# Optimization experiments

Hardware: AMD Instinct MI355X
Metric: run time of the kernel (lower is better)

## Reference

```python
import jax, jax.numpy as jnp
import numpy as np

N_NODES = 100000
N_EDGES = 300000
N_GRAPHS = 128
NODE_VOCAB = 200
NODE_DIM = 128
EDGE_VOCAB = 8
EDGE_DIM = 64
K_LAYERS = 3


def setup_inputs() -> dict:
    key = jax.random.key(0)
    ks = iter(jax.random.split(key, 40))
    f = lambda shape: jax.random.normal(next(ks), shape, dtype=jnp.float32)
    s = lambda shape: f(shape) * 0.05
    inp = {}
    inp["x_s"] = f((N_NODES, NODE_VOCAB))
    inp["x_t"] = f((N_NODES, NODE_VOCAB))
    inp["edge_attr_s"] = f((2 * N_EDGES, EDGE_VOCAB))
    inp["edge_attr_t"] = f((2 * N_EDGES, EDGE_VOCAB))
    inp["edge_index_s"] = jax.random.randint(next(ks), (2, N_EDGES), 0, N_NODES)
    inp["edge_index_t"] = jax.random.randint(next(ks), (2, N_EDGES), 0, N_NODES)
    inp["x_s_batch"] = jnp.sort(jax.random.randint(next(ks), (N_NODES,), 0, N_GRAPHS))
    inp["x_t_batch"] = jnp.sort(jax.random.randint(next(ks), (N_NODES,), 0, N_GRAPHS))
    inp["y"] = jax.random.randint(next(ks), (N_GRAPHS,), 0, 2)
    cat = 2 * NODE_DIM + EDGE_DIM  # 320: [x_src, edge_attr, x_dst]
    inp["node_emb"] = s((NODE_VOCAB, NODE_DIM))
    inp["edge_emb"] = s((EDGE_VOCAB, EDGE_DIM))
    inp["W_in_0"] = s((K_LAYERS, cat, EDGE_DIM))
    inp["W_in_1"] = s((K_LAYERS, EDGE_DIM, 1))
    inp["W_out_0"] = s((K_LAYERS, cat, EDGE_DIM))
    inp["W_out_1"] = s((K_LAYERS, EDGE_DIM, 1))
    inp["Wg_in"] = s((K_LAYERS, NODE_DIM, NODE_DIM))
    inp["bg_in"] = jnp.zeros((K_LAYERS, NODE_DIM), jnp.float32)
    inp["Wg_out"] = s((K_LAYERS, NODE_DIM, NODE_DIM))
    inp["bg_out"] = jnp.zeros((K_LAYERS, NODE_DIM), jnp.float32)
    inp["cls_W0"] = s((2 * NODE_DIM, NODE_DIM))
    inp["cls_b0"] = jnp.zeros((NODE_DIM,), jnp.float32)
    inp["cls_W1"] = s((NODE_DIM, 2))
    inp["cls_b1"] = jnp.zeros((2,), jnp.float32)
    return inp


def _dag_embed(x, e, row, col, W_in_0, W_in_1, W_out_0, W_out_1, Wg_in, bg_in, Wg_out, bg_out):
    N = x.shape[0]
    E = row.shape[0]
    for k in range(W_in_0.shape[0]):
        e_in, e_out = e[:E], e[E:]  # chunk(edge_attr_x, 2, dim=0)
        info_in = jnp.concatenate([x[row], e_in, x[col]], axis=1)   # [E, 2D+Ce]
        info_out = jnp.concatenate([x[col], e_out, x[row]], axis=1)
        e_in = info_in @ W_in_0[k]
        e_out = info_out @ W_out_0[k]
        w_in = jax.nn.sigmoid(e_in @ W_in_1[k]).ravel()   # [E]
        w_out = jax.nn.sigmoid(e_out @ W_out_1[k]).ravel()
        # embedding_in: flow source->target (x_j = x[row], aggregate at col)
        xi = x @ Wg_in[k]
        x_in = jax.ops.segment_sum(w_in[:, None] * xi[row], col, num_segments=N) + bg_in[k]
        # embedding_out: flow target->source (x_j = x[col], aggregate at row)
        xo = x @ Wg_out[k]
        x_out = jax.ops.segment_sum(w_out[:, None] * xo[col], row, num_segments=N) + bg_out[k]
        x = x + x_in + x_out
        e = jnp.concatenate([e_in, e_out], axis=0)
    return x


def _mean_pool(x, batch, num_graphs):
    sums = jax.ops.segment_sum(x, batch, num_segments=num_graphs)
    cnt = jax.ops.segment_sum(jnp.ones((x.shape[0], 1), x.dtype), batch, num_segments=num_graphs)
    return sums / jnp.maximum(cnt, 1.0)


def reference(x_s, x_t, edge_attr_s, edge_attr_t, edge_index_s, edge_index_t,
              x_s_batch, x_t_batch, y, node_emb, edge_emb,
              W_in_0, W_in_1, W_out_0, W_out_1, Wg_in, bg_in, Wg_out, bg_out,
              cls_W0, cls_b0, cls_W1, cls_b1):
    # Initialization: argmax -> embedding lookup
    h_s = node_emb[jnp.argmax(x_s, axis=1)]
    h_t = node_emb[jnp.argmax(x_t, axis=1)]
    he_s = edge_emb[jnp.argmax(edge_attr_s, axis=1)]
    he_t = edge_emb[jnp.argmax(edge_attr_t, axis=1)]
    h_s = _dag_embed(h_s, he_s, edge_index_s[0], edge_index_s[1],
                     W_in_0, W_in_1, W_out_0, W_out_1, Wg_in, bg_in, Wg_out, bg_out)
    h_t = _dag_embed(h_t, he_t, edge_index_t[0], edge_index_t[1],
                     W_in_0, W_in_1, W_out_0, W_out_1, Wg_in, bg_in, Wg_out, bg_out)
    g_s = _mean_pool(h_s, x_s_batch, N_GRAPHS)
    g_t = _mean_pool(h_t, x_t_batch, N_GRAPHS)
    h = jax.nn.relu(jnp.concatenate([g_s, g_t], axis=1) @ cls_W0 + cls_b0)
    logits = h @ cls_W1 + cls_b1
    logp = jax.nn.log_softmax(logits, axis=1)
    loss = -jnp.mean(jnp.take_along_axis(logp, y[:, None], axis=1))
    return loss
```

## Files before the change

kernel.cpp:

```cpp
#include <hip/hip_runtime.h>
#include <hip/hip_bf16.h>

#define N_NODES 100000
#define N_EDGES 300000
#define N_GRAPHS 128
#define NODE_VOCAB 200
#define NODE_DIM 128
#define EDGE_DIM 64
#define K_LAYERS 3

#define SCAN_CHUNK 2048
#define SCAN_NBLK ((N_NODES + SCAN_CHUNK - 1) / SCAN_CHUNK)

typedef unsigned short ushort_t;
typedef __attribute__((ext_vector_type(8))) __bf16 bf16x8;
typedef __attribute__((ext_vector_type(4))) float f32x4;

__device__ inline ushort_t f2bf(float f) {
    unsigned int u = __float_as_uint(f);
    unsigned int r = (u + 0x7fff + ((u >> 16) & 1)) >> 16;
    return (ushort_t)r;
}
__device__ inline float bf2f(ushort_t u) {
    return __uint_as_float(((unsigned int)u) << 16);
}
__device__ inline float bflo(unsigned int u) { return __uint_as_float(u << 16); }
__device__ inline float bfhi(unsigned int u) { return __uint_as_float(u & 0xffff0000u); }

#define MASK_J0 0x15151515u
#define MASK_J1 0x28282828u
#define MASK_J2 0x40404040u

__device__ ushort_t g_hb[2][(size_t)N_NODES * NODE_DIM];
__device__ ushort_t g_XWx_b[(size_t)N_NODES * 256];
__device__ ushort_t g_WcatT[256 * 128];
__device__ ushort_t g_QT[K_LAYERS][32][128];
__device__ float g_scal[(size_t)N_NODES * 32];
__device__ float g_bias[8][6];
__device__ int  g_evoc[2 * N_EDGES];
__device__ float g_gsum[2][N_GRAPHS * NODE_DIM];
__device__ float g_cnt[2][N_GRAPHS];
__device__ float g_H[N_GRAPHS * NODE_DIM];
__device__ int  g_deg_in[N_NODES];
__device__ int  g_deg_out[N_NODES];
__device__ int  g_off_in[N_NODES + 1];
__device__ int  g_off_out[N_NODES + 1];
__device__ int  g_cur_in[N_NODES];
__device__ int  g_cur_out[N_NODES];
__device__ int2 g_lst_in[N_EDGES];
__device__ int2 g_lst_out[N_EDGES];
__device__ int  g_bsum[2][SCAN_NBLK];
__device__ int  g_boff[2][SCAN_NBLK];

__global__ void node_embed_kernel(const float* __restrict__ x, const float* __restrict__ emb,
                                  int N) {
    int wave = threadIdx.x >> 6;
    int lane = threadIdx.x & 63;
    int n = blockIdx.x * 4 + wave;
    if (n >= N) return;
    const float* xr = x + (size_t)n * NODE_VOCAB;
    float v = xr[lane];
    int idx = lane;
    float nv = xr[lane + 64];
    if (nv > v) { v = nv; idx = lane + 64; }
    nv = xr[lane + 128];
    if (nv > v) { v = nv; idx = lane + 128; }
    if (lane < NODE_VOCAB - 192) {
        nv = xr[lane + 192];
        if (nv > v) { v = nv; idx = lane + 192; }
    }
    #pragma unroll
    for (int off = 32; off; off >>= 1) {
        float ov = __shfl_xor(v, off);
        int oi = __shfl_xor(idx, off);
        if (ov > v || (ov == v && oi < idx)) { v = ov; idx = oi; }
    }
    const float* er = emb + (size_t)idx * NODE_DIM;
    g_hb[0][(size_t)n * NODE_DIM + lane] = f2bf(er[lane]);
    g_hb[0][(size_t)n * NODE_DIM + 64 + lane] = f2bf(er[64 + lane]);
}

__global__ void edge_voc_kernel(const float* __restrict__ ea, int M) {
    long idx = (long)blockIdx.x * 256 + threadIdx.x;
    if (idx >= M) return;
    const float* ar = ea + idx * 8;
    float4 v0 = *(const float4*)ar;
    float4 v1 = *(const float4*)(ar + 4);
    float vals[8] = {v0.x, v0.y, v0.z, v0.w, v1.x, v1.y, v1.z, v1.w};
    int best = 0;
    float bv = vals[0];
    #pragma unroll
    for (int i = 1; i < 8; ++i)
        if (vals[i] > bv) { bv = vals[i]; best = i; }
    g_evoc[idx] = best;
}

__global__ void zero_qt_kernel() {
    int i = blockIdx.x * 256 + threadIdx.x;
    if (i < K_LAYERS * 32 * 128) ((ushort_t*)g_QT)[i] = 0;
}

__global__ void setup_gates_kernel(const float* __restrict__ Wi0, const float* __restrict__ Wi1,
                                   const float* __restrict__ Wo0, const float* __restrict__ Wo1,
                                   const float* __restrict__ eemb) {
    int b = blockIdx.x;
    int D = b / 3, k = b % 3;
    int t = threadIdx.x;
    const float* W0 = D ? Wo0 : Wi0;
    const float* W1 = D ? Wo1 : Wi1;
    __shared__ float u[64], un[64];
    if (t < 64) u[t] = W1[k * 64 + t];
    __syncthreads();
    int offk = (k == 0) ? 0 : (k == 1 ? 2 : 4);
    for (int j = k; j >= 0; --j) {
        const float* Wj = W0 + (size_t)j * 320 * 64;
        float qa = 0.f, qc = 0.f;
        for (int m = 0; m < 64; ++m) {
            float um = u[m];
            qa += Wj[t * 64 + m] * um;
            qc += Wj[(192 + t) * 64 + m] * um;
        }
        g_QT[j][(D ? 8 : 0) + offk + j][t] = f2bf(qa);
        g_QT[j][(D ? 24 : 16) + offk + j][t] = f2bf(qc);
        float s = 0.f;
        if (t < 64) {
            for (int m = 0; m < 64; ++m) s += Wj[(128 + t) * 64 + m] * u[m];
        }
        __syncthreads();
        if (t < 64) un[t] = s;
        __syncthreads();
        if (t < 64) u[t] = un[t];
        __syncthreads();
    }
    if (t < 8) {
        float s = 0.f;
        for (int m = 0; m < 64; ++m) s += eemb[t * 64 + m] * u[m];
        g_bias[t][D * 3 + k] = s;
    }
}

__global__ void csr_zero_kernel() {
    int i = blockIdx.x * 256 + threadIdx.x;
    if (i < N_NODES) { g_deg_in[i] = 0; g_deg_out[i] = 0; }
}

__global__ void csr_count_kernel(const int* __restrict__ row, const int* __restrict__ col,
                                 int E) {
    int e = blockIdx.x * 256 + threadIdx.x;
    if (e >= E) return;
    atomicAdd(&g_deg_in[col[e]], 1);
    atomicAdd(&g_deg_out[row[e]], 1);
}

__global__ void csr_bsum_kernel() {
    int which = blockIdx.y;
    const int* deg = which ? g_deg_out : g_deg_in;
    int b = blockIdx.x;
    int t = threadIdx.x;
    int base = b * SCAN_CHUNK;
    int s = 0;
    #pragma unroll
    for (int i = 0; i < SCAN_CHUNK / 256; ++i) {
        int idx = base + i * 256 + t;
        if (idx < N_NODES) s += deg[idx];
    }
    __shared__ int red[256];
    red[t] = s;
    __syncthreads();
    for (int d = 128; d; d >>= 1) {
        if (t < d) red[t] += red[t + d];
        __syncthreads();
    }
    if (t == 0) g_bsum[which][b] = red[0];
}

__global__ void csr_bscan_kernel() {
    int which = blockIdx.x;
    int t = threadIdx.x;
    int v = (t < SCAN_NBLK) ? g_bsum[which][t] : 0;
    int orig = v;
    #pragma unroll
    for (int d = 1; d < 64; d <<= 1) {
        int u = __shfl_up(v, d, 64);
        if (t >= d) v += u;
    }
    if (t < SCAN_NBLK) g_boff[which][t] = v - orig;
}

__global__ void csr_off_kernel(int total) {
    int which = blockIdx.y;
    const int* deg = which ? g_deg_out : g_deg_in;
    int* off = which ? g_off_out : g_off_in;
    int* cur = which ? g_cur_out : g_cur_in;
    int b = blockIdx.x;
    int t = threadIdx.x;
    const int per = SCAN_CHUNK / 256;
    int lo = b * SCAN_CHUNK + t * per;
    int d8[per];
    int s = 0;
    #pragma unroll
    for (int i = 0; i < per; ++i) {
        int idx = lo + i;
        d8[i] = (idx < N_NODES) ? deg[idx] : 0;
        s += d8[i];
    }
    __shared__ int part[256];
    part[t] = s;
    __syncthreads();
    for (int d = 1; d < 256; d <<= 1) {
        int add = (t >= d) ? part[t - d] : 0;
        __syncthreads();
        part[t] += add;
        __syncthreads();
    }
    int run = g_boff[which][b] + part[t] - s;
    #pragma unroll
    for (int i = 0; i < per; ++i) {
        int idx = lo + i;
        if (idx < N_NODES) {
            off[idx] = run;
            cur[idx] = run;
            run += d8[i];
        }
    }
    if (b == 0 && t == 0) off[N_NODES] = total;
}

__global__ void csr_fill_kernel(const int* __restrict__ row, const int* __restrict__ col,
                                int E) {
    int e = blockIdx.x * 256 + threadIdx.x;
    if (e >= E) return;
    int r = row[e], c = col[e];
    int p = atomicAdd(&g_cur_in[c], 1);
    g_lst_in[p] = make_int2(r, g_evoc[e]);
    int q = atomicAdd(&g_cur_out[r], 1);
    g_lst_out[q] = make_int2(c, g_evoc[E + e]);
}

__global__ void assemble_wcat(const float* __restrict__ Wgi, const float* __restrict__ Wgo) {
    int idx = blockIdx.x * 256 + threadIdx.x;
    int n = idx >> 7;
    int kd = idx & 127;
    float v = (n < 128) ? Wgi[kd * 128 + n] : Wgo[kd * 128 + (n - 128)];
    g_WcatT[n * 128 + kd] = f2bf(v);
}

__global__ __launch_bounds__(320) void gemm_xw_mfma(int cur, int layer, unsigned int mask,
                                                    int M) {
    const ushort_t* __restrict__ hb = g_hb[cur];
    int m0 = blockIdx.x * 64;
    int t = threadIdx.x;
    int wave = t >> 6, lane = t & 63;
    __shared__ ushort_t As[64 * 128];

    for (int idx = t; idx < 1024; idx += 320) {
        int m = idx >> 4, c = idx & 15;
        int gm = m0 + m;
        uint4 v = make_uint4(0u, 0u, 0u, 0u);
        if (gm < M) v = *(const uint4*)(hb + (size_t)gm * 128 + c * 8);
        *(uint4*)&As[m * 128 + ((c * 8) ^ ((m & 7) << 3))] = v;
    }
    __syncthreads();

    int lr = lane & 15, lk = lane >> 4;

    if (wave < 4) {
        int nbase = wave * 64;
        f32x4 acc[4][4];
        #pragma unroll
        for (int i = 0; i < 4; ++i)
            #pragma unroll
            for (int j = 0; j < 4; ++j)
                acc[i][j] = (f32x4){0.f, 0.f, 0.f, 0.f};

        const ushort_t* Bbase = g_WcatT + (size_t)nbase * 128;
        #pragma unroll
        for (int ks = 0; ks < 4; ++ks) {
            bf16x8 a[4], b[4];
            int ke = ks * 32 + lk * 8;
            #pragma unroll
            for (int mt = 0; mt < 4; ++mt) {
                int row = mt * 16 + lr;
                a[mt] = *(const bf16x8*)&As[row * 128 + (ke ^ ((row & 7) << 3))];
            }
            #pragma unroll
            for (int nt = 0; nt < 4; ++nt) {
                b[nt] = *(const bf16x8*)(Bbase + (size_t)(nt * 16 + lr) * 128 + ke);
            }
            #pragma unroll
            for (int nt = 0; nt < 4; ++nt)
                #pragma unroll
                for (int mt = 0; mt < 4; ++mt)
                    acc[nt][mt] = __builtin_amdgcn_mfma_f32_16x16x32_bf16(b[nt], a[mt], acc[nt][mt], 0, 0, 0);
        }

        #pragma unroll
        for (int mt = 0; mt < 4; ++mt) {
            int gm = m0 + mt * 16 + lr;
            if (gm >= M) continue;
            #pragma unroll
            for (int nt = 0; nt < 4; ++nt) {
                int n0 = nbase + nt * 16 + lk * 4;
                f32x4 av = acc[nt][mt];
                uint2 pk;
                pk.x = ((unsigned int)f2bf(av[1]) << 16) | (unsigned int)f2bf(av[0]);
                pk.y = ((unsigned int)f2bf(av[3]) << 16) | (unsigned int)f2bf(av[2]);
                *(uint2*)&g_XWx_b[(size_t)gm * 256 + n0] = pk;
            }
        }
    } else {
        const ushort_t* QT = &g_QT[layer][0][0];
        f32x4 acc[2][4];
        #pragma unroll
        for (int i = 0; i < 2; ++i)
            #pragma unroll
            for (int j = 0; j < 4; ++j)
                acc[i][j] = (f32x4){0.f, 0.f, 0.f, 0.f};

        #pragma unroll
        for (int ks = 0; ks < 4; ++ks) {
            bf16x8 a[4], b[2];
            int ke = ks * 32 + lk * 8;
            #pragma unroll
            for (int mt = 0; mt < 4; ++mt) {
                int row = mt * 16 + lr;
                a[mt] = *(const bf16x8*)&As[row * 128 + (ke ^ ((row & 7) << 3))];
            }
            #pragma unroll
            for (int nt = 0; nt < 2; ++nt)
                b[nt] = *(const bf16x8*)&QT[(nt * 16 + lr) * 128 + ke];
            #pragma unroll
            for (int nt = 0; nt < 2; ++nt)
                #pragma unroll
                for (int mt = 0; mt < 4; ++mt)
                    acc[nt][mt] = __builtin_amdgcn_mfma_f32_16x16x32_bf16(b[nt], a[mt], acc[nt][mt], 0, 0, 0);
        }

        #pragma unroll
        for (int mt = 0; mt < 4; ++mt) {
            int gm = m0 + mt * 16 + lr;
            if (gm >= M) continue;
            #pragma unroll
            for (int nt = 0; nt < 2; ++nt) {
                #pragma unroll
                for (int r = 0; r < 4; ++r) {
                    int colc = nt * 16 + lk * 4 + r;
                    if ((mask >> colc) & 1u)
                        g_scal[(size_t)gm * 32 + colc] = acc[nt][mt][r];
                }
            }
        }
    }
}

__global__ __launch_bounds__(256) void aggregate_kernel(int cur, int k,
                                                        const float* __restrict__ bgi,
                                                        const float* __restrict__ bgo, int N) {
    __shared__ float sW[4][64];
    __shared__ int sS[4][64];
    int wv = threadIdx.x >> 6;
    int lane = threadIdx.x & 63;
    int grp = lane >> 4, li = lane & 15;
    int n = blockIdx.x * 4 + wv;
    if (n >= N) return;
    float bias_in = g_bias[lane & 7][k];
    float bias_out = g_bias[lane & 7][3 + k];
    const float* srow = g_scal + (size_t)n * 32;
    float cin, cout;
    if (k == 0) {
        cin = srow[16]; cout = srow[24];
    } else if (k == 1) {
        cin = srow[18] + srow[19]; cout = srow[26] + srow[27];
    } else {
        cin = srow[20] + srow[21] + srow[22];
        cout = srow[28] + srow[29] + srow[30];
    }
    int pin0 = g_off_in[n], din = g_off_in[n + 1] - pin0;
    int pout0 = g_off_out[n], dout = g_off_out[n + 1] - pout0;
    int tot = din + dout;

    float acc[8];
    if (grp == 0) {
        uint4 xv = *(const uint4*)(g_hb[cur] + (size_t)n * 128 + li * 8);
        float4 b1 = *(const float4*)(bgi + li * 8);
        float4 b2 = *(const float4*)(bgi + li * 8 + 4);
        float4 c1 = *(const float4*)(bgo + li * 8);
        float4 c2 = *(const float4*)(bgo + li * 8 + 4);
        acc[0] = bflo(xv.x) + b1.x + c1.x;
        acc[1] = bfhi(xv.x) + b1.y + c1.y;
        acc[2] = bflo(xv.y) + b1.z + c1.z;
        acc[3] = bfhi(xv.y) + b1.w + c1.w;
        acc[4] = bflo(xv.z) + b2.x + c2.x;
        acc[5] = bfhi(xv.z) + b2.y + c2.y;
        acc[6] = bflo(xv.w) + b2.z + c2.z;
        acc[7] = bfhi(xv.w) + b2.w + c2.w;
    } else {
        #pragma unroll
        for (int q = 0; q < 8; ++q) acc[q] = 0.f;
    }

    for (int base = 0; base < tot; base += 64) {
        int cnt = min(64, tot - base);
        if (lane < cnt) {
            int q = base + lane;
            int2 se;
            int dir;
            if (q < din) { se = g_lst_in[pin0 + q]; dir = 0; }
            else         { se = g_lst_out[pout0 + q - din]; dir = 1; }
            const float* arow = g_scal + (size_t)se.x * 32 + dir * 8;
            float asum;
            if (k == 0) asum = arow[0];
            else if (k == 1) asum = arow[2] + arow[3];
            else asum = arow[4] + arow[5] + arow[6];
            float bi = __shfl(bias_in, se.y);
            float bo = __shfl(bias_out, se.y);
            float s = (dir ? bo : bi) + asum + (dir ? cout : cin);
            sW[wv][lane] = 1.0f / (1.0f + __expf(-s));
            sS[wv][lane] = se.x * 2 + dir;
        }
        for (int e = grp; e < cnt; e += 4) {
            float wvv = sW[wv][e];
            int sv = sS[wv][e];
            const ushort_t* src = g_XWx_b + (size_t)(sv >> 1) * 256 + (sv & 1) * 128 + li * 8;
            uint4 pv = *(const uint4*)src;
            acc[0] += wvv * bflo(pv.x);
            acc[1] += wvv * bfhi(pv.x);
            acc[2] += wvv * bflo(pv.y);
            acc[3] += wvv * bfhi(pv.y);
            acc[4] += wvv * bflo(pv.z);
            acc[5] += wvv * bfhi(pv.z);
            acc[6] += wvv * bflo(pv.w);
            acc[7] += wvv * bfhi(pv.w);
        }
    }
    #pragma unroll
    for (int q = 0; q < 8; ++q) {
        acc[q] += __shfl_xor(acc[q], 16);
        acc[q] += __shfl_xor(acc[q], 32);
    }
    if (grp == 0) {
        uint4 pk;
        pk.x = ((unsigned int)f2bf(acc[1]) << 16) | (unsigned int)f2bf(acc[0]);
        pk.y = ((unsigned int)f2bf(acc[3]) << 16) | (unsigned int)f2bf(acc[2]);
        pk.z = ((unsigned int)f2bf(acc[5]) << 16) | (unsigned int)f2bf(acc[4]);
        pk.w = ((unsigned int)f2bf(acc[7]) << 16) | (unsigned int)f2bf(acc[6]);
        *(uint4*)(g_hb[cur ^ 1] + (size_t)n * 128 + li * 8) = pk;
    }
}

__global__ void pool_kernel(int fin, int side, const int* __restrict__ batch, int N) {
    const ushort_t* x = g_hb[fin];
    float* gsum = g_gsum[side];
    int n0 = blockIdx.x * 128;
    int d = threadIdx.x;
    if (n0 >= N) return;
    int nend = min(n0 + 128, N);
    float acc = 0.f;
    int curg = batch[n0];
    for (int n = n0; n < nend; ++n) {
        int g = batch[n];
        if (g != curg) {
            atomicAdd(&gsum[curg * 128 + d], acc);
            acc = 0.f;
            curg = g;
        }
        acc += bf2f(x[(size_t)n * 128 + d]);
    }
    atomicAdd(&gsum[curg * 128 + d], acc);
}

__global__ void count_kernel(int side, const int* __restrict__ batch, int N) {
    int g = threadIdx.x;
    int lo = 0, hi = N;
    while (lo < hi) { int mid = (lo + hi) >> 1; if (batch[mid] < g) lo = mid + 1; else hi = mid; }
    int a = lo;
    lo = 0; hi = N;
    while (lo < hi) { int mid = (lo + hi) >> 1; if (batch[mid] < g + 1) lo = mid + 1; else hi = mid; }
    g_cnt[side][g] = (float)(lo - a);
}

__global__ void zero_gsum_kernel() {
    int i = blockIdx.x * 256 + threadIdx.x;
    if (i < 2 * N_GRAPHS * NODE_DIM) ((float*)g_gsum)[i] = 0.f;
}

__global__ void hidden_kernel(const float* __restrict__ W0, const float* __restrict__ b0) {
    int g = blockIdx.x;
    int j = threadIdx.x;
    float inv_s = 1.0f / fmaxf(g_cnt[0][g], 1.0f);
    float inv_t = 1.0f / fmaxf(g_cnt[1][g], 1.0f);
    float acc = b0[j];
    for (int k = 0; k < 128; ++k) acc += g_gsum[0][g * 128 + k] * inv_s * W0[k * 128 + j];
    for (int k = 0; k < 128; ++k) acc += g_gsum[1][g * 128 + k] * inv_t * W0[(128 + k) * 128 + j];
    g_H[g * 128 + j] = fmaxf(acc, 0.f);
}

__global__ void loss_kernel(const float* __restrict__ W1, const float* __restrict__ b1,
                            const int* __restrict__ y, float* __restrict__ out) {
    int g = threadIdx.x;
    float l0 = b1[0], l1 = b1[1];
    for (int j = 0; j < 128; ++j) {
        float hv = g_H[g * 128 + j];
        l0 += hv * W1[j * 2 + 0];
        l1 += hv * W1[j * 2 + 1];
    }
    float m = fmaxf(l0, l1);
    float lse = m + logf(expf(l0 - m) + expf(l1 - m));
    float ly = (y[g] == 0) ? l0 : l1;
    float c = -(ly - lse) * (1.0f / (float)N_GRAPHS);
    __shared__ float red[128];
    red[g] = c;
    __syncthreads();
    for (int s = 64; s; s >>= 1) {
        if (g < s) red[g] += red[g + s];
        __syncthreads();
    }
    if (g == 0) out[0] = red[0];
}

extern "C" void kernel_launch(void* const* d_in, const int* in_sizes, int n_in,
                              void* d_out, int out_size, void* d_ws, size_t ws_size,
                              hipStream_t stream) {
    const float* x_s      = (const float*)d_in[0];
    const float* x_t      = (const float*)d_in[1];
    const float* ea_s     = (const float*)d_in[2];
    const float* ea_t     = (const float*)d_in[3];
    const int*   ei_s     = (const int*)d_in[4];
    const int*   ei_t     = (const int*)d_in[5];
    const int*   batch_s  = (const int*)d_in[6];
    const int*   batch_t  = (const int*)d_in[7];
    const int*   y        = (const int*)d_in[8];
    const float* node_emb = (const float*)d_in[9];
    const float* edge_emb = (const float*)d_in[10];
    const float* W_in_0   = (const float*)d_in[11];
    const float* W_in_1   = (const float*)d_in[12];
    const float* W_out_0  = (const float*)d_in[13];
    const float* W_out_1  = (const float*)d_in[14];
    const float* Wg_in    = (const float*)d_in[15];
    const float* bg_in    = (const float*)d_in[16];
    const float* Wg_out   = (const float*)d_in[17];
    const float* bg_out   = (const float*)d_in[18];
    const float* cls_W0   = (const float*)d_in[19];
    const float* cls_b0   = (const float*)d_in[20];
    const float* cls_W1   = (const float*)d_in[21];
    const float* cls_b1   = (const float*)d_in[22];

    const int N = N_NODES, E = N_EDGES;
    static const unsigned int MASKS[3] = {MASK_J0, MASK_J1, MASK_J2};

    zero_gsum_kernel<<<(2 * N_GRAPHS * NODE_DIM + 255) / 256, 256, 0, stream>>>();
    zero_qt_kernel<<<(K_LAYERS * 32 * 128 + 255) / 256, 256, 0, stream>>>();
    setup_gates_kernel<<<6, 128, 0, stream>>>(W_in_0, W_in_1, W_out_0, W_out_1, edge_emb);

    for (int side = 0; side < 2; ++side) {
        const float* xin   = side ? x_t : x_s;
        const float* eain  = side ? ea_t : ea_s;
        const int*   ei    = side ? ei_t : ei_s;
        const int*   batch = side ? batch_t : batch_s;
        const int* row = ei;
        const int* col = ei + E;

        node_embed_kernel<<<(N + 3) / 4, 256, 0, stream>>>(xin, node_emb, N);
        edge_voc_kernel<<<(2 * E + 255) / 256, 256, 0, stream>>>(eain, 2 * E);

        csr_zero_kernel<<<(N + 255) / 256, 256, 0, stream>>>();
        csr_count_kernel<<<(E + 255) / 256, 256, 0, stream>>>(row, col, E);
        csr_bsum_kernel<<<dim3(SCAN_NBLK, 2), 256, 0, stream>>>();
        csr_bscan_kernel<<<2, 64, 0, stream>>>();
        csr_off_kernel<<<dim3(SCAN_NBLK, 2), 256, 0, stream>>>(E);
        csr_fill_kernel<<<(E + 255) / 256, 256, 0, stream>>>(row, col, E);

        int cur = 0;
        for (int k = 0; k < K_LAYERS; ++k) {
            assemble_wcat<<<128, 256, 0, stream>>>(Wg_in + (size_t)k * 128 * 128,
                                                   Wg_out + (size_t)k * 128 * 128);
            gemm_xw_mfma<<<(N + 63) / 64, 320, 0, stream>>>(cur, k, MASKS[k], N);
            aggregate_kernel<<<(N + 3) / 4, 256, 0, stream>>>(
                cur, k, bg_in + (size_t)k * 128, bg_out + (size_t)k * 128, N);
            cur ^= 1;
        }
        pool_kernel<<<(N + 127) / 128, 128, 0, stream>>>(cur, side, batch, N);
        count_kernel<<<1, 128, 0, stream>>>(side, batch, N);
    }

    hidden_kernel<<<128, 128, 0, stream>>>(cls_W0, cls_b0);
    loss_kernel<<<1, 128, 0, stream>>>(cls_W1, cls_b1, y, (float*)d_out);
}
```

Measured before the change: 922.4 us.

## Map one node per 16-lane group in aggregation and hoist weight assembly

The aggregation kernel now gives each node a 16-lane group instead of a whole wavefront, so four nodes share one wave. Gates are computed per lane and broadcast with shuffles instead of going through shared memory, and the final cross-group reduction goes away. The Wcat transpose for all layers is also built once up front rather than re-launched per layer and per side. The aim is better lane use on low-degree nodes and fewer launches, at the cost of divergence when node degrees differ within a wave.

```diff
diff --git a/kernel.cpp b/kernel.cpp
--- a/kernel.cpp
+++ b/kernel.cpp
@@ -33,7 +33,7 @@
 
 __device__ ushort_t g_hb[2][(size_t)N_NODES * NODE_DIM];
 __device__ ushort_t g_XWx_b[(size_t)N_NODES * 256];
-__device__ ushort_t g_WcatT[256 * 128];
+__device__ ushort_t g_WcatT[K_LAYERS][256 * 128];
 __device__ ushort_t g_QT[K_LAYERS][32][128];
 __device__ float g_scal[(size_t)N_NODES * 32];
 __device__ float g_bias[8][6];
@@ -237,12 +237,16 @@
     g_lst_out[q] = make_int2(c, g_evoc[E + e]);
 }
 
-__global__ void assemble_wcat(const float* __restrict__ Wgi, const float* __restrict__ Wgo) {
+__global__ void assemble_wcat_all(const float* __restrict__ Wgi, const float* __restrict__ Wgo) {
     int idx = blockIdx.x * 256 + threadIdx.x;
-    int n = idx >> 7;
-    int kd = idx & 127;
-    float v = (n < 128) ? Wgi[kd * 128 + n] : Wgo[kd * 128 + (n - 128)];
-    g_WcatT[n * 128 + kd] = f2bf(v);
+    if (idx >= K_LAYERS * 32768) return;
+    int k = idx >> 15;
+    int rem = idx & 32767;
+    int n = rem >> 7;
+    int kd = rem & 127;
+    float v = (n < 128) ? Wgi[(size_t)k * 16384 + kd * 128 + n]
+                        : Wgo[(size_t)k * 16384 + kd * 128 + (n - 128)];
+    g_WcatT[k][n * 128 + kd] = f2bf(v);
 }
 
 __global__ __launch_bounds__(320) void gemm_xw_mfma(int cur, int layer, unsigned int mask,
@@ -273,7 +277,7 @@
             for (int j = 0; j < 4; ++j)
                 acc[i][j] = (f32x4){0.f, 0.f, 0.f, 0.f};
 
-        const ushort_t* Bbase = g_WcatT + (size_t)nbase * 128;
+        const ushort_t* Bbase = &g_WcatT[layer][0] + (size_t)nbase * 128;
         #pragma unroll
         for (int ks = 0; ks < 4; ++ks) {
             bf16x8 a[4], b[4];
@@ -356,36 +360,38 @@
 __global__ __launch_bounds__(256) void aggregate_kernel(int cur, int k,
                                                         const float* __restrict__ bgi,
                                                         const float* __restrict__ bgo, int N) {
-    __shared__ float sW[4][64];
-    __shared__ int sS[4][64];
-    int wv = threadIdx.x >> 6;
-    int lane = threadIdx.x & 63;
+    int tid = threadIdx.x;
+    int wv = tid >> 6;
+    int lane = tid & 63;
     int grp = lane >> 4, li = lane & 15;
-    int n = blockIdx.x * 4 + wv;
-    if (n >= N) return;
-    float bias_in = g_bias[lane & 7][k];
-    float bias_out = g_bias[lane & 7][3 + k];
-    const float* srow = g_scal + (size_t)n * 32;
-    float cin, cout;
-    if (k == 0) {
-        cin = srow[16]; cout = srow[24];
-    } else if (k == 1) {
-        cin = srow[18] + srow[19]; cout = srow[26] + srow[27];
-    } else {
-        cin = srow[20] + srow[21] + srow[22];
-        cout = srow[28] + srow[29] + srow[30];
-    }
-    int pin0 = g_off_in[n], din = g_off_in[n + 1] - pin0;
-    int pout0 = g_off_out[n], dout = g_off_out[n + 1] - pout0;
+    int n = blockIdx.x * 16 + wv * 4 + grp;
+    bool valid = n < N;
+
+    int pin0 = 0, din = 0, pout0 = 0, dout = 0;
+    float cin = 0.f, cout = 0.f;
+    if (valid) {
+        pin0 = g_off_in[n];  din = g_off_in[n + 1] - pin0;
+        pout0 = g_off_out[n]; dout = g_off_out[n + 1] - pout0;
+        const float* srow = g_scal + (size_t)n * 32;
+        if (k == 0) {
+            cin = srow[16]; cout = srow[24];
+        } else if (k == 1) {
+            cin = srow[18] + srow[19]; cout = srow[26] + srow[27];
+        } else {
+            cin = srow[20] + srow[21] + srow[22];
+            cout = srow[28] + srow[29] + srow[30];
+        }
+    }
     int tot = din + dout;
 
     float acc[8];
-    if (grp == 0) {
-        uint4 xv = *(const uint4*)(g_hb[cur] + (size_t)n * 128 + li * 8);
+    {
         float4 b1 = *(const float4*)(bgi + li * 8);
         float4 b2 = *(const float4*)(bgi + li * 8 + 4);
         float4 c1 = *(const float4*)(bgo + li * 8);
         float4 c2 = *(const float4*)(bgo + li * 8 + 4);
+        uint4 xv = make_uint4(0u, 0u, 0u, 0u);
+        if (valid) xv = *(const uint4*)(g_hb[cur] + (size_t)n * 128 + li * 8);
         acc[0] = bflo(xv.x) + b1.x + c1.x;
         acc[1] = bfhi(xv.x) + b1.y + c1.y;
         acc[2] = bflo(xv.y) + b1.z + c1.z;
@@ -394,15 +400,14 @@
         acc[5] = bfhi(xv.z) + b2.y + c2.y;
         acc[6] = bflo(xv.w) + b2.z + c2.z;
         acc[7] = bfhi(xv.w) + b2.w + c2.w;
-    } else {
-        #pragma unroll
-        for (int q = 0; q < 8; ++q) acc[q] = 0.f;
-    }
-
-    for (int base = 0; base < tot; base += 64) {
-        int cnt = min(64, tot - base);
-        if (lane < cnt) {
-            int q = base + lane;
+    }
+
+    for (int base = 0; base < tot; base += 16) {
+        int cnt = min(16, tot - base);
+        float gate = 0.f;
+        int sv = 0;
+        if (li < cnt) {
+            int q = base + li;
             int2 se;
             int dir;
             if (q < din) { se = g_lst_in[pin0 + q]; dir = 0; }
@@ -412,17 +417,14 @@
             if (k == 0) asum = arow[0];
             else if (k == 1) asum = arow[2] + arow[3];
             else asum = arow[4] + arow[5] + arow[6];
-            float bi = __shfl(bias_in, se.y);
-            float bo = __shfl(bias_out, se.y);
-            float s = (dir ? bo : bi) + asum + (dir ? cout : cin);
-            sW[wv][lane] = 1.0f / (1.0f + __expf(-s));
-            sS[wv][lane] = se.x * 2 + dir;
-        }
-        for (int e = grp; e < cnt; e += 4) {
-            float wvv = sW[wv][e];
-            int sv = sS[wv][e];
-            const ushort_t* src = g_XWx_b + (size_t)(sv >> 1) * 256 + (sv & 1) * 128 + li * 8;
-            uint4 pv = *(const uint4*)src;
+            float s = g_bias[se.y][dir * 3 + k] + asum + (dir ? cout : cin);
+            gate = 1.0f / (1.0f + __expf(-s));
+            sv = se.x * 2 + dir;
+        }
+        for (int e = 0; e < cnt; ++e) {
+            float wvv = __shfl(gate, grp * 16 + e);
+            int s2 = __shfl(sv, grp * 16 + e);
+            uint4 pv = *(const uint4*)(g_XWx_b + (size_t)(s2 >> 1) * 256 + (s2 & 1) * 128 + li * 8);
             acc[0] += wvv * bflo(pv.x);
             acc[1] += wvv * bfhi(pv.x);
             acc[2] += wvv * bflo(pv.y);
@@ -433,12 +435,8 @@
             acc[7] += wvv * bfhi(pv.w);
         }
     }
-    #pragma unroll
-    for (int q = 0; q < 8; ++q) {
-        acc[q] += __shfl_xor(acc[q], 16);
-        acc[q] += __shfl_xor(acc[q], 32);
-    }
-    if (grp == 0) {
+
+    if (valid) {
         uint4 pk;
         pk.x = ((unsigned int)f2bf(acc[1]) << 16) | (unsigned int)f2bf(acc[0]);
         pk.y = ((unsigned int)f2bf(acc[3]) << 16) | (unsigned int)f2bf(acc[2]);
@@ -551,6 +549,7 @@
     zero_gsum_kernel<<<(2 * N_GRAPHS * NODE_DIM + 255) / 256, 256, 0, stream>>>();
     zero_qt_kernel<<<(K_LAYERS * 32 * 128 + 255) / 256, 256, 0, stream>>>();
     setup_gates_kernel<<<6, 128, 0, stream>>>(W_in_0, W_in_1, W_out_0, W_out_1, edge_emb);
+    assemble_wcat_all<<<(K_LAYERS * 32768 + 255) / 256, 256, 0, stream>>>(Wg_in, Wg_out);
 
     for (int side = 0; side < 2; ++side) {
         const float* xin   = side ? x_t : x_s;
@@ -572,10 +571,8 @@
 
         int cur = 0;
         for (int k = 0; k < K_LAYERS; ++k) {
-            assemble_wcat<<<128, 256, 0, stream>>>(Wg_in + (size_t)k * 128 * 128,
-                                                   Wg_out + (size_t)k * 128 * 128);
             gemm_xw_mfma<<<(N + 63) / 64, 320, 0, stream>>>(cur, k, MASKS[k], N);
-            aggregate_kernel<<<(N + 3) / 4, 256, 0, stream>>>(
+            aggregate_kernel<<<(N + 15) / 16, 256, 0, stream>>>(
                 cur, k, bg_in + (size_t)k * 128, bg_out + (size_t)k * 128, N);
             cur ^= 1;
         }
```

New measurement: 899.1 us. 2.5% less time.
